# Performance work log

Hardware: AMD Instinct MI355X
Metric: run time of the kernel (lower is better)

Reference implementation:

```python
import jax, jax.numpy as jnp
import numpy as np

N = 100000   # nodes
E = 1600000  # edges
H = 150      # hidden_dim
G = 256      # num graphs in batch
L = 5        # num_layers
GATE_H = 200


def setup_inputs() -> dict:
    key = jax.random.key(0)
    ks = jax.random.split(key, 12)
    s = lambda k, shape, fan: jax.random.normal(k, shape, dtype=jnp.float32) / np.sqrt(fan)
    return {
        "x": jax.random.normal(ks[0], (N, H), dtype=jnp.float32),
        "edge_index": jax.random.randint(ks[1], (2, E), 0, N, dtype=jnp.int64),
        "batch": jnp.sort(jax.random.randint(ks[2], (N,), 0, G, dtype=jnp.int64)),
        "W": s(ks[3], (L, H, H), H),              # GatedGraphConv per-layer weight
        "w_ih": s(ks[4], (3 * H, H), H),           # GRUCell input weights (r,z,n)
        "w_hh": s(ks[5], (3 * H, H), H),
        "b_ih": jnp.zeros((3 * H,), jnp.float32),
        "b_hh": jnp.zeros((3 * H,), jnp.float32),
        "gw1": s(ks[6], (H, GATE_H), H),           # gate_nn Linear(150,200)
        "gb1": jnp.zeros((GATE_H,), jnp.float32),
        "gw2": s(ks[7], (GATE_H, 1), GATE_H),      # gate_nn Linear(200,1)
        "gb2": jnp.zeros((1,), jnp.float32),
    }


def _gru_cell(m, h, w_ih, w_hh, b_ih, b_hh):
    gi = m @ w_ih.T + b_ih   # [N, 3H]
    gh = h @ w_hh.T + b_hh
    ir, iz, inn = jnp.split(gi, 3, axis=-1)
    hr, hz, hn = jnp.split(gh, 3, axis=-1)
    r = jax.nn.sigmoid(ir + hr)
    z = jax.nn.sigmoid(iz + hz)
    n = jnp.tanh(inn + r * hn)
    return (1.0 - z) * n + z * h


def reference(x, edge_index, batch, W, w_ih, w_hh, b_ih, b_hh, gw1, gb1, gw2, gb2):
    src, dst = edge_index[0], edge_index[1]
    h = x
    # GatedGraphConv: per layer, linear transform, scatter_add aggregation, GRU update
    for i in range(L):
        m = h @ W[i]                                   # [N, H]
        agg = jax.ops.segment_sum(m[src], dst, num_segments=N)  # scatter_add over edges
        h = _gru_cell(agg, h, w_ih, w_hh, b_ih, b_hh)
    # GlobalAttention readout
    gate = jnp.tanh(h @ gw1 + gb1) @ gw2 + gb2          # [N, 1]
    gmax = jax.ops.segment_max(gate, batch, num_segments=G)    # [G, 1]
    gate = jnp.exp(gate - gmax[batch])
    gsum = jax.ops.segment_sum(gate, batch, num_segments=G)    # [G, 1]
    gate = gate / (gsum[batch] + 1e-16)                 # segment softmax
    out = jax.ops.segment_sum(gate * h, batch, num_segments=G)  # [G, H]
    return out, gate
```

## Files before the change

kernel.cpp:

```cpp
#include <hip/hip_runtime.h>
#include <math.h>

#define NN 100000
#define NE 1600000
#define H 150
#define NG 256
#define NL 5
#define GH 200
#define HS 160
#define LS 168
#define CHN 1563
#define SNB 98

typedef unsigned short u16;
typedef unsigned int   u32;
typedef __attribute__((ext_vector_type(8))) short bf16x8;
typedef __attribute__((ext_vector_type(4))) float f32x4;

__device__ __forceinline__ float bf2f(u32 lo16){ u32 t = lo16 << 16; return __builtin_bit_cast(float, t); }
__device__ __forceinline__ u16 f2bf(float f){
  u32 u = __builtin_bit_cast(u32, f);
  u += 0x7fffu + ((u >> 16) & 1u);
  return (u16)(u >> 16);
}
__device__ __forceinline__ u32 pack2(float a, float b){ return (u32)f2bf(a) | ((u32)f2bf(b) << 16); }
__device__ __forceinline__ float fast_sig(float x){
  float e = __expf(-x);
  return __builtin_amdgcn_rcpf(1.f + e);
}
__device__ __forceinline__ float fast_tanh(float x){
  float cx = fminf(fmaxf(x, -15.f), 15.f);
  float e = __expf(2.f*cx);
  return (e - 1.f) * __builtin_amdgcn_rcpf(e + 1.f);
}

__global__ void k_hist(const int* __restrict__ ed, int* __restrict__ cnt){
  int e = blockIdx.x*256 + threadIdx.x;
  if (e < NE) atomicAdd(&cnt[ed[e]], 1);
}

__global__ __launch_bounds__(256) void k_scan1(const int* __restrict__ cnt, int* __restrict__ part){
  __shared__ int red[256];
  const int b = blockIdx.x, tid = threadIdx.x;
  const int base = b*1024;
  int s = 0;
  #pragma unroll
  for (int i = 0; i < 4; ++i){
    int idx = base + tid + i*256;
    s += (idx < NN) ? cnt[idx] : 0;
  }
  red[tid] = s; __syncthreads();
  for (int st = 128; st >= 1; st >>= 1){
    if (tid < st) red[tid] += red[tid+st];
    __syncthreads();
  }
  if (tid == 0) part[b] = red[0];
}

__global__ void k_scan2(int* __restrict__ part){
  const int t = threadIdx.x;
  int v0 = (2*t   < SNB) ? part[2*t]   : 0;
  int v1 = (2*t+1 < SNB) ? part[2*t+1] : 0;
  int s = v0 + v1, x = s;
  #pragma unroll
  for (int off = 1; off < 64; off <<= 1){
    int tt = __shfl_up(x, off);
    if (t >= off) x += tt;
  }
  int excl = x - s;
  if (2*t   < SNB) part[2*t]   = excl;
  if (2*t+1 < SNB) part[2*t+1] = excl + v0;
}

__global__ __launch_bounds__(1024) void k_scan3(const int* __restrict__ cnt,
        const int* __restrict__ part, int* __restrict__ rowptr, int* __restrict__ cursor){
  __shared__ int wsum[16];
  const int b = blockIdx.x, tid = threadIdx.x;
  const int wid = tid >> 6, lane = tid & 63;
  const int idx = b*1024 + tid;
  int v = (idx < NN) ? cnt[idx] : 0;
  int x = v;
  #pragma unroll
  for (int off = 1; off < 64; off <<= 1){
    int t = __shfl_up(x, off);
    if (lane >= off) x += t;
  }
  if (lane == 63) wsum[wid] = x;
  __syncthreads();
  if (tid < 16){
    int s = wsum[tid];
    int y = s;
    #pragma unroll
    for (int off = 1; off < 16; off <<= 1){
      int t = __shfl_up(y, off);
      if (tid >= off) y += t;
    }
    wsum[tid] = y - s;
  }
  __syncthreads();
  if (idx < NN){
    int incl = part[b] + wsum[wid] + x;
    rowptr[idx+1] = incl;
    cursor[idx]   = incl - v;
  }
  if (idx == 0) rowptr[0] = 0;
}

__global__ void k_fill(const int* __restrict__ es, const int* __restrict__ ed,
                       int* __restrict__ cursor, int* __restrict__ csr){
  int e = blockIdx.x*256 + threadIdx.x;
  if (e < NE){
    int pos = atomicAdd(&cursor[ed[e]], 1);
    csr[pos] = es[e];
  }
}

__global__ __launch_bounds__(256) void k_wc(const float* __restrict__ W,
        const float* __restrict__ wih, float* __restrict__ Wc){
  int idx = blockIdx.x*256 + threadIdx.x;
  if (idx >= NL*H*450) return;
  int l = idx / (H*450);
  int rem = idx - l*H*450;
  int k = rem / 450;
  int j = rem - k*450;
  const float* Wr = W   + (size_t)l*H*H + (size_t)k*H;
  const float* wr = wih + (size_t)j*H;
  float acc = 0.f;
  for (int t = 0; t < H; ++t) acc = fmaf(Wr[t], wr[t], acc);
  Wc[idx] = acc;
}

__global__ void k_packi(const float* __restrict__ Wc, short* __restrict__ wbi){
  int idx = blockIdx.x*256 + threadIdx.x;
  int li = idx & 511;
  int q = idx >> 9;
  int mat = q % 3; q /= 3;
  int ks = q % 5;  q /= 5;
  int ct = q % 10; int l = q / 10;
  int lane = li >> 3, j = li & 7;
  int k = ks*32 + ((lane >> 4) << 3) + j;
  int col = ct*16 + (lane & 15);
  float v = (k < H && col < H) ? Wc[(size_t)l*H*450 + (size_t)k*450 + mat*H + col] : 0.f;
  wbi[idx] = (short)f2bf(v);
}

__global__ void k_packh(const float* __restrict__ whh, short* __restrict__ wbh){
  int idx = blockIdx.x*256 + threadIdx.x;
  int li = idx & 511;
  int q = idx >> 9;
  int mat = q % 3; q /= 3;
  int ks = q % 5;  int ct = q / 5;
  int lane = li >> 3, j = li & 7;
  int k = ks*32 + ((lane >> 4) << 3) + j;
  int col = ct*16 + (lane & 15);
  float v = (k < H && col < H) ? whh[(size_t)(mat*H + col)*H + k] : 0.f;
  wbh[idx] = (short)f2bf(v);
}

__global__ void k_packg(const float* __restrict__ gw1, short* __restrict__ gw1b){
  int idx = blockIdx.x*256 + threadIdx.x;
  int li = idx & 511;
  int q = idx >> 9;
  int ks = q % 5;  int ct = q / 5;
  int lane = li >> 3, j = li & 7;
  int k = ks*32 + ((lane >> 4) << 3) + j;
  int col = ct*16 + (lane & 15);
  float v = (k < H && col < GH) ? gw1[(size_t)k*GH + col] : 0.f;
  gw1b[idx] = (short)f2bf(v);
}

__global__ void k_cvt(const float* __restrict__ x, short* __restrict__ hb){
  int idx = blockIdx.x*256 + threadIdx.x;
  if (idx >= NN*80) return;
  int n = idx / 80, c2 = idx - n*80;
  int c = c2*2;
  float lo = (c   < H) ? x[(size_t)n*H + c]   : 0.f;
  float hi = (c+1 < H) ? x[(size_t)n*H + c+1] : 0.f;
  ((u32*)hb)[idx] = (u32)f2bf(lo) | ((u32)f2bf(hi) << 16);
}

__global__ __launch_bounds__(256) void k_gather(const short* __restrict__ hb,
        const int* __restrict__ rowptr, const int* __restrict__ csr,
        short* __restrict__ aggb){
  const int lane = threadIdx.x & 63;
  const int n = blockIdx.x*4 + (threadIdx.x >> 6);
  if (n >= NN) return;
  const int s0 = rowptr[n], s1 = rowptr[n+1];
  const u32* h32 = (const u32*)hb;
  const bool ext = lane < 16;
  float x0=0.f, x1=0.f, y0=0.f, y1=0.f;
  int j = s0;
  for (; j + 3 < s1; j += 4){
    const u32* r0 = h32 + (size_t)csr[j]*80;
    const u32* r1 = h32 + (size_t)csr[j+1]*80;
    const u32* r2 = h32 + (size_t)csr[j+2]*80;
    const u32* r3 = h32 + (size_t)csr[j+3]*80;
    u32 v0 = r0[lane], v1 = r1[lane], v2 = r2[lane], v3 = r3[lane];
    u32 u0=0,u1=0,u2=0,u3=0;
    if (ext){ u0 = r0[64+lane]; u1 = r1[64+lane]; u2 = r2[64+lane]; u3 = r3[64+lane]; }
    x0 += bf2f(v0 & 0xffffu) + bf2f(v1 & 0xffffu) + bf2f(v2 & 0xffffu) + bf2f(v3 & 0xffffu);
    x1 += bf2f(v0 >> 16)     + bf2f(v1 >> 16)     + bf2f(v2 >> 16)     + bf2f(v3 >> 16);
    if (ext){
      y0 += bf2f(u0 & 0xffffu) + bf2f(u1 & 0xffffu) + bf2f(u2 & 0xffffu) + bf2f(u3 & 0xffffu);
      y1 += bf2f(u0 >> 16)     + bf2f(u1 >> 16)     + bf2f(u2 >> 16)     + bf2f(u3 >> 16);
    }
  }
  for (; j < s1; ++j){
    const u32* r0 = h32 + (size_t)csr[j]*80;
    u32 v0 = r0[lane];
    x0 += bf2f(v0 & 0xffffu); x1 += bf2f(v0 >> 16);
    if (ext){
      u32 u0 = r0[64+lane];
      y0 += bf2f(u0 & 0xffffu); y1 += bf2f(u0 >> 16);
    }
  }
  u32* o = (u32*)aggb + (size_t)n*80;
  o[lane] = pack2(x0, x1);
  if (ext) o[64+lane] = pack2(y0, y1);
}

__global__ __launch_bounds__(256, 2) void k_gru(
    const short* __restrict__ aggb, const short* __restrict__ hbc,
    short* __restrict__ hbn,
    const short* __restrict__ wbi_l, const short* __restrict__ wbh,
    const float* __restrict__ bih, const float* __restrict__ bhh){
  __shared__ short sA[64*LS];
  __shared__ short sH[64*LS];
  __shared__ short sB[30*512];
  const int tid = threadIdx.x;
  const int w = tid >> 6, lane = tid & 63;
  const int l16 = lane & 15, g = lane >> 4, g8 = g*8;
  const int row0 = blockIdx.x*64;

  for (int i = tid; i < 64*20; i += 256){
    int r = i/20, c = i - r*20;
    int gr = row0 + r;
    bf16x8 va = {0,0,0,0,0,0,0,0}, vh = {0,0,0,0,0,0,0,0};
    if (gr < NN){
      va = *(const bf16x8*)&aggb[(size_t)gr*HS + c*8];
      vh = *(const bf16x8*)&hbc [(size_t)gr*HS + c*8];
    }
    *(bf16x8*)&sA[r*LS + c*8] = va;
    *(bf16x8*)&sH[r*LS + c*8] = vh;
  }

  bf16x8 pr[8];
  #pragma unroll
  for (int k2 = 0; k2 < 8; ++k2){
    int u = tid + k2*256;
    if (u < 1920){
      int s = u >> 6, e = u & 63;
      const short* src = (s < 15) ? (wbi_l + s*512 + e*8)
                                  : (wbh  + (s-15)*512 + e*8);
      pr[k2] = *(const bf16x8*)src;
    }
  }

  for (int ct = 0; ct < 10; ++ct){
    __syncthreads();
    #pragma unroll
    for (int k2 = 0; k2 < 8; ++k2){
      int u = tid + k2*256;
      if (u < 1920) *(bf16x8*)&sB[u*8] = pr[k2];
    }
    __syncthreads();
    if (ct < 9){
      const int cto = (ct+1)*7680;
      #pragma unroll
      for (int k2 = 0; k2 < 8; ++k2){
        int u = tid + k2*256;
        if (u < 1920){
          int s = u >> 6, e = u & 63;
          const short* src = (s < 15) ? (wbi_l + cto + s*512 + e*8)
                                      : (wbh  + cto + (s-15)*512 + e*8);
          pr[k2] = *(const bf16x8*)src;
        }
      }
    }

    const int col = ct*16 + l16;
    const bool cv = col < H;
    float bir = cv ? bih[col] : 0.f, biz = cv ? bih[H+col] : 0.f, bin_ = cv ? bih[2*H+col] : 0.f;
    float bhr = cv ? bhh[col] : 0.f, bhz = cv ? bhh[H+col] : 0.f, bhn  = cv ? bhh[2*H+col] : 0.f;

    f32x4 a0={0,0,0,0},a1={0,0,0,0},a2={0,0,0,0},a3={0,0,0,0},a4={0,0,0,0},a5={0,0,0,0};
    const int lr = w*16 + l16;
    #pragma unroll
    for (int ks = 0; ks < 5; ++ks){
      bf16x8 aA = *(const bf16x8*)&sA[lr*LS + ks*32 + g8];
      bf16x8 aH = *(const bf16x8*)&sH[lr*LS + ks*32 + g8];
      bf16x8 b0 = *(const bf16x8*)&sB[(ks*3+0)*512 + lane*8];
      bf16x8 b1 = *(const bf16x8*)&sB[(ks*3+1)*512 + lane*8];
      bf16x8 b2 = *(const bf16x8*)&sB[(ks*3+2)*512 + lane*8];
      bf16x8 c0 = *(const bf16x8*)&sB[(15+ks*3+0)*512 + lane*8];
      bf16x8 c1 = *(const bf16x8*)&sB[(15+ks*3+1)*512 + lane*8];
      bf16x8 c2 = *(const bf16x8*)&sB[(15+ks*3+2)*512 + lane*8];
      a0 = __builtin_amdgcn_mfma_f32_16x16x32_bf16(aA, b0, a0, 0,0,0);
      a1 = __builtin_amdgcn_mfma_f32_16x16x32_bf16(aA, b1, a1, 0,0,0);
      a2 = __builtin_amdgcn_mfma_f32_16x16x32_bf16(aA, b2, a2, 0,0,0);
      a3 = __builtin_amdgcn_mfma_f32_16x16x32_bf16(aH, c0, a3, 0,0,0);
      a4 = __builtin_amdgcn_mfma_f32_16x16x32_bf16(aH, c1, a4, 0,0,0);
      a5 = __builtin_amdgcn_mfma_f32_16x16x32_bf16(aH, c2, a5, 0,0,0);
    }
    if (cv){
      #pragma unroll
      for (int r = 0; r < 4; ++r){
        int lrow = w*16 + g*4 + r;
        int grow = row0 + lrow;
        if (grow < NN){
          float rr = fast_sig(a0[r]+bir + a3[r]+bhr);
          float zz = fast_sig(a1[r]+biz + a4[r]+bhz);
          float nn = fast_tanh(a2[r]+bin_ + rr*(a5[r]+bhn));
          float hold = bf2f((u32)(u16)sH[lrow*LS + col]);
          float hnew = (1.f-zz)*nn + zz*hold;
          hbn[(size_t)grow*HS + col] = (short)f2bf(hnew);
        }
      }
    }
  }
}

__global__ __launch_bounds__(256) void k_gatepre(const short* __restrict__ hb,
      const short* __restrict__ gw1b, const float* __restrict__ gb1,
      const float* __restrict__ gw2, const float* __restrict__ gb2,
      float* __restrict__ gbuf){
  __shared__ short sh[64*LS];
  __shared__ float part[4][4][4][4];
  const int tid = threadIdx.x;
  const int w = tid >> 6, lane = tid & 63;
  const int l16 = lane & 15, g = lane >> 4, g8 = g*8;
  const int chunk = blockIdx.x, row0 = chunk*64;

  for (int i = tid; i < 64*20; i += 256){
    int r = i/20, c = i - r*20;
    int gr = row0 + r;
    bf16x8 v = {0,0,0,0,0,0,0,0};
    if (gr < NN) v = *(const bf16x8*)&hb[(size_t)gr*HS + c*8];
    *(bf16x8*)&sh[r*LS + c*8] = v;
  }
  __syncthreads();

  float acc[4][4];
  #pragma unroll
  for (int rt=0; rt<4; ++rt){
    #pragma unroll
    for (int r=0; r<4; ++r) acc[rt][r] = 0.f;
  }
  for (int ct = w; ct < 13; ct += 4){
    bf16x8 B[5];
    const short* p = gw1b + (size_t)(ct*5)*512 + lane*8;
    #pragma unroll
    for (int ks = 0; ks < 5; ++ks) B[ks] = *(const bf16x8*)&p[ks*512];
    int col = ct*16 + l16;
    bool cv = col < GH;
    float g2 = cv ? gw2[col] : 0.f;
    float b1 = cv ? gb1[col] : 0.f;
    #pragma unroll
    for (int rt = 0; rt < 4; ++rt){
      f32x4 d = {0,0,0,0};
      #pragma unroll
      for (int ks = 0; ks < 5; ++ks){
        bf16x8 aH = *(const bf16x8*)&sh[(rt*16 + l16)*LS + ks*32 + g8];
        d = __builtin_amdgcn_mfma_f32_16x16x32_bf16(aH, B[ks], d, 0,0,0);
      }
      if (cv){
        #pragma unroll
        for (int r = 0; r < 4; ++r) acc[rt][r] += fast_tanh(d[r] + b1) * g2;
      }
    }
  }
  #pragma unroll
  for (int rt = 0; rt < 4; ++rt){
    #pragma unroll
    for (int r = 0; r < 4; ++r){
      float v = acc[rt][r];
      v += __shfl_xor(v, 1); v += __shfl_xor(v, 2);
      v += __shfl_xor(v, 4); v += __shfl_xor(v, 8);
      if (l16 == 0) part[w][rt][g][r] = v;
    }
  }
  __syncthreads();
  if (tid < 64){
    int rt = tid >> 4, gg = (tid >> 2) & 3, r = tid & 3;
    int grow = row0 + tid;
    if (grow < NN)
      gbuf[grow] = part[0][rt][gg][r] + part[1][rt][gg][r]
                 + part[2][rt][gg][r] + part[3][rt][gg][r] + gb2[0];
  }
}

__global__ __launch_bounds__(256) void k_readout(float* __restrict__ gatebuf,
    const short* __restrict__ hb, const int* __restrict__ batch,
    float* __restrict__ out, float* __restrict__ gate_out){
  const int g = blockIdx.x;
  const int tid = threadIdx.x;
  int lo=0, hi=NN;
  while (lo<hi){ int mid=(lo+hi)>>1; if (batch[mid] < g) lo=mid+1; else hi=mid; }
  const int start = lo;
  hi = NN;
  while (lo<hi){ int mid=(lo+hi)>>1; if (batch[mid] < g+1) lo=mid+1; else hi=mid; }
  const int end = lo;

  __shared__ float red[256];
  __shared__ float s_max, s_inv;
  float mx = -INFINITY;
  for (int n = start+tid; n < end; n += 256) mx = fmaxf(mx, gatebuf[n]);
  red[tid]=mx; __syncthreads();
  for (int s=128; s>=1; s>>=1){ if (tid<s) red[tid]=fmaxf(red[tid],red[tid+s]); __syncthreads(); }
  if (tid==0) s_max = red[0];
  __syncthreads();
  const float gmax = s_max;
  float sum = 0.f;
  for (int n = start+tid; n < end; n += 256){
    float e = expf(gatebuf[n]-gmax);
    gatebuf[n] = e;
    sum += e;
  }
  red[tid]=sum; __syncthreads();
  for (int s=128; s>=1; s>>=1){ if (tid<s) red[tid]+=red[tid+s]; __syncthreads(); }
  if (tid==0) s_inv = 1.0f/(red[0] + 1e-16f);
  __syncthreads();
  const float inv = s_inv;
  for (int n = start+tid; n < end; n += 256) gate_out[n] = gatebuf[n]*inv;
  if (tid < 80){
    const u32* h32 = (const u32*)hb;
    float acc0 = 0.f, acc1 = 0.f;
    for (int n = start; n < end; ++n){
      u32 v = h32[(size_t)n*80 + tid];
      float gv = gatebuf[n];
      acc0 = fmaf(gv, bf2f(v & 0xffffu), acc0);
      acc1 = fmaf(gv, bf2f(v >> 16),     acc1);
    }
    int c0 = 2*tid, c1 = 2*tid + 1;
    if (c0 < H) out[g*H + c0] = acc0*inv;
    if (c1 < H) out[g*H + c1] = acc1*inv;
  }
}

extern "C" void kernel_launch(void* const* d_in, const int* in_sizes, int n_in,
                              void* d_out, int out_size, void* d_ws, size_t ws_size,
                              hipStream_t stream) {
  (void)in_sizes; (void)n_in; (void)out_size; (void)ws_size;
  const float* x    = (const float*)d_in[0];
  const int*   eidx = (const int*)d_in[1];
  const int*   batch= (const int*)d_in[2];
  const float* W    = (const float*)d_in[3];
  const float* wih  = (const float*)d_in[4];
  const float* whh  = (const float*)d_in[5];
  const float* bih  = (const float*)d_in[6];
  const float* bhh  = (const float*)d_in[7];
  const float* gw1  = (const float*)d_in[8];
  const float* gb1  = (const float*)d_in[9];
  const float* gw2  = (const float*)d_in[10];
  const float* gb2  = (const float*)d_in[11];

  float* out      = (float*)d_out;
  float* gate_out = out + NG*H;

  char* p = (char*)d_ws;
  float* gbuf  = (float*)p;  p += (size_t)NN*4;
  float* Wc    = (float*)p;  p += (size_t)NL*H*450*4;
  short* hb0   = (short*)p;  p += (size_t)NN*HS*2;
  short* hb1   = (short*)p;  p += (size_t)NN*HS*2;
  short* aggb  = (short*)p;  p += (size_t)NN*HS*2;
  short* wbi   = (short*)p;  p += (size_t)NL*76800*2;
  short* wbh   = (short*)p;  p += (size_t)76800*2;
  short* gw1b  = (short*)p;  p += (size_t)33280*2;
  int*   cnt   = (int*)p;    p += (size_t)NN*4;
  int*   rowptr= (int*)p;    p += (size_t)(NN+1)*4;
  int*   cursor= (int*)p;    p += (size_t)NN*4;
  int*   csr   = (int*)p;    p += (size_t)NE*4;
  int*   spart = (int*)p;    p += (size_t)SNB*4;

  const int* esrc = eidx;
  const int* edst = eidx + NE;

  hipMemsetAsync(cnt, 0, sizeof(int)*NN, stream);
  k_hist<<<(NE+255)/256, 256, 0, stream>>>(edst, cnt);
  k_scan1<<<SNB, 256, 0, stream>>>(cnt, spart);
  k_scan2<<<1, 64, 0, stream>>>(spart);
  k_scan3<<<SNB, 1024, 0, stream>>>(cnt, spart, rowptr, cursor);
  k_fill<<<(NE+255)/256, 256, 0, stream>>>(esrc, edst, cursor, csr);

  k_wc   <<<(NL*H*450+255)/256, 256, 0, stream>>>(W, wih, Wc);
  k_packi<<<1500, 256, 0, stream>>>(Wc, wbi);
  k_packh<<<300,  256, 0, stream>>>(whh, wbh);
  k_packg<<<130,  256, 0, stream>>>(gw1, gw1b);

  k_cvt<<<(NN*80+255)/256, 256, 0, stream>>>(x, hb0);

  for (int l = 0; l < NL; ++l){
    short* cur  = (l & 1) ? hb1 : hb0;
    short* next = (l & 1) ? hb0 : hb1;
    k_gather<<<NN/4, 256, 0, stream>>>(cur, rowptr, csr, aggb);
    k_gru<<<CHN, 256, 0, stream>>>(aggb, cur, next,
                                   wbi + (size_t)l*76800, wbh, bih, bhh);
  }
  k_gatepre<<<CHN, 256, 0, stream>>>(hb1, gw1b, gb1, gw2, gb2, gbuf);
  k_readout<<<NG, 256, 0, stream>>>(gbuf, hb1, batch, out, gate_out);
}
```

Before: 1.307 ms.

## Keep GRU A-fragments in registers with 128-row tiles; unroll gather by eight

The GRU kernel no longer stages aggregated and hidden tiles in shared memory. Each wave loads its own MFMA A-fragments straight from global memory into registers and covers 32 rows instead of 16. Each weight tile staged in LDS is therefore reused for twice as many rows, and the grid is halved. The old hidden value is now re-read from global memory in the epilogue. The gather kernel's neighbour loop is unrolled from 4 to 8 to keep more loads in flight. Register pressure rises in both kernels, which may lower occupancy.

```diff
diff --git a/kernel.cpp b/kernel.cpp
--- a/kernel.cpp
+++ b/kernel.cpp
@@ -10,6 +10,7 @@
 #define HS 160
 #define LS 168
 #define CHN 1563
+#define CH2 782
 #define SNB 98
 
 typedef unsigned short u16;
@@ -190,19 +191,31 @@
   const bool ext = lane < 16;
   float x0=0.f, x1=0.f, y0=0.f, y1=0.f;
   int j = s0;
-  for (; j + 3 < s1; j += 4){
+  for (; j + 7 < s1; j += 8){
     const u32* r0 = h32 + (size_t)csr[j]*80;
     const u32* r1 = h32 + (size_t)csr[j+1]*80;
     const u32* r2 = h32 + (size_t)csr[j+2]*80;
     const u32* r3 = h32 + (size_t)csr[j+3]*80;
+    const u32* r4 = h32 + (size_t)csr[j+4]*80;
+    const u32* r5 = h32 + (size_t)csr[j+5]*80;
+    const u32* r6 = h32 + (size_t)csr[j+6]*80;
+    const u32* r7 = h32 + (size_t)csr[j+7]*80;
     u32 v0 = r0[lane], v1 = r1[lane], v2 = r2[lane], v3 = r3[lane];
-    u32 u0=0,u1=0,u2=0,u3=0;
-    if (ext){ u0 = r0[64+lane]; u1 = r1[64+lane]; u2 = r2[64+lane]; u3 = r3[64+lane]; }
-    x0 += bf2f(v0 & 0xffffu) + bf2f(v1 & 0xffffu) + bf2f(v2 & 0xffffu) + bf2f(v3 & 0xffffu);
-    x1 += bf2f(v0 >> 16)     + bf2f(v1 >> 16)     + bf2f(v2 >> 16)     + bf2f(v3 >> 16);
+    u32 v4 = r4[lane], v5 = r5[lane], v6 = r6[lane], v7 = r7[lane];
+    u32 u0=0,u1=0,u2=0,u3=0,u4=0,u5=0,u6=0,u7=0;
     if (ext){
-      y0 += bf2f(u0 & 0xffffu) + bf2f(u1 & 0xffffu) + bf2f(u2 & 0xffffu) + bf2f(u3 & 0xffffu);
-      y1 += bf2f(u0 >> 16)     + bf2f(u1 >> 16)     + bf2f(u2 >> 16)     + bf2f(u3 >> 16);
+      u0 = r0[64+lane]; u1 = r1[64+lane]; u2 = r2[64+lane]; u3 = r3[64+lane];
+      u4 = r4[64+lane]; u5 = r5[64+lane]; u6 = r6[64+lane]; u7 = r7[64+lane];
+    }
+    x0 += bf2f(v0 & 0xffffu) + bf2f(v1 & 0xffffu) + bf2f(v2 & 0xffffu) + bf2f(v3 & 0xffffu)
+        + bf2f(v4 & 0xffffu) + bf2f(v5 & 0xffffu) + bf2f(v6 & 0xffffu) + bf2f(v7 & 0xffffu);
+    x1 += bf2f(v0 >> 16) + bf2f(v1 >> 16) + bf2f(v2 >> 16) + bf2f(v3 >> 16)
+        + bf2f(v4 >> 16) + bf2f(v5 >> 16) + bf2f(v6 >> 16) + bf2f(v7 >> 16);
+    if (ext){
+      y0 += bf2f(u0 & 0xffffu) + bf2f(u1 & 0xffffu) + bf2f(u2 & 0xffffu) + bf2f(u3 & 0xffffu)
+          + bf2f(u4 & 0xffffu) + bf2f(u5 & 0xffffu) + bf2f(u6 & 0xffffu) + bf2f(u7 & 0xffffu);
+      y1 += bf2f(u0 >> 16) + bf2f(u1 >> 16) + bf2f(u2 >> 16) + bf2f(u3 >> 16)
+          + bf2f(u4 >> 16) + bf2f(u5 >> 16) + bf2f(u6 >> 16) + bf2f(u7 >> 16);
     }
   }
   for (; j < s1; ++j){
@@ -224,24 +237,26 @@
     short* __restrict__ hbn,
     const short* __restrict__ wbi_l, const short* __restrict__ wbh,
     const float* __restrict__ bih, const float* __restrict__ bhh){
-  __shared__ short sA[64*LS];
-  __shared__ short sH[64*LS];
   __shared__ short sB[30*512];
   const int tid = threadIdx.x;
   const int w = tid >> 6, lane = tid & 63;
   const int l16 = lane & 15, g = lane >> 4, g8 = g*8;
-  const int row0 = blockIdx.x*64;
-
-  for (int i = tid; i < 64*20; i += 256){
-    int r = i/20, c = i - r*20;
-    int gr = row0 + r;
-    bf16x8 va = {0,0,0,0,0,0,0,0}, vh = {0,0,0,0,0,0,0,0};
-    if (gr < NN){
-      va = *(const bf16x8*)&aggb[(size_t)gr*HS + c*8];
-      vh = *(const bf16x8*)&hbc [(size_t)gr*HS + c*8];
-    }
-    *(bf16x8*)&sA[r*LS + c*8] = va;
-    *(bf16x8*)&sH[r*LS + c*8] = vh;
+  const int row0 = blockIdx.x*128 + w*32;
+
+  bf16x8 fA[2][5], fH[2][5];
+  #pragma unroll
+  for (int t = 0; t < 2; ++t){
+    const int r = row0 + t*16 + l16;
+    const bool rv = r < NN;
+    #pragma unroll
+    for (int ks = 0; ks < 5; ++ks){
+      bf16x8 va = {0,0,0,0,0,0,0,0}, vh = {0,0,0,0,0,0,0,0};
+      if (rv){
+        va = *(const bf16x8*)&aggb[(size_t)r*HS + ks*32 + g8];
+        vh = *(const bf16x8*)&hbc [(size_t)r*HS + ks*32 + g8];
+      }
+      fA[t][ks] = va; fH[t][ks] = vh;
+    }
   }
 
   bf16x8 pr[8];
@@ -280,40 +295,48 @@
 
     const int col = ct*16 + l16;
     const bool cv = col < H;
-    float bir = cv ? bih[col] : 0.f, biz = cv ? bih[H+col] : 0.f, bin_ = cv ? bih[2*H+col] : 0.f;
-    float bhr = cv ? bhh[col] : 0.f, bhz = cv ? bhh[H+col] : 0.f, bhn  = cv ? bhh[2*H+col] : 0.f;
-
-    f32x4 a0={0,0,0,0},a1={0,0,0,0},a2={0,0,0,0},a3={0,0,0,0},a4={0,0,0,0},a5={0,0,0,0};
-    const int lr = w*16 + l16;
+    const float bir = cv ? bih[col] : 0.f, biz = cv ? bih[H+col] : 0.f, bin_ = cv ? bih[2*H+col] : 0.f;
+    const float bhr = cv ? bhh[col] : 0.f, bhz = cv ? bhh[H+col] : 0.f, bhn  = cv ? bhh[2*H+col] : 0.f;
+
+    f32x4 ai[2][3], ah[2][3];
+    #pragma unroll
+    for (int t = 0; t < 2; ++t)
+      #pragma unroll
+      for (int m = 0; m < 3; ++m){ ai[t][m] = (f32x4){0,0,0,0}; ah[t][m] = (f32x4){0,0,0,0}; }
+
     #pragma unroll
     for (int ks = 0; ks < 5; ++ks){
-      bf16x8 aA = *(const bf16x8*)&sA[lr*LS + ks*32 + g8];
-      bf16x8 aH = *(const bf16x8*)&sH[lr*LS + ks*32 + g8];
-      bf16x8 b0 = *(const bf16x8*)&sB[(ks*3+0)*512 + lane*8];
-      bf16x8 b1 = *(const bf16x8*)&sB[(ks*3+1)*512 + lane*8];
-      bf16x8 b2 = *(const bf16x8*)&sB[(ks*3+2)*512 + lane*8];
-      bf16x8 c0 = *(const bf16x8*)&sB[(15+ks*3+0)*512 + lane*8];
-      bf16x8 c1 = *(const bf16x8*)&sB[(15+ks*3+1)*512 + lane*8];
-      bf16x8 c2 = *(const bf16x8*)&sB[(15+ks*3+2)*512 + lane*8];
-      a0 = __builtin_amdgcn_mfma_f32_16x16x32_bf16(aA, b0, a0, 0,0,0);
-      a1 = __builtin_amdgcn_mfma_f32_16x16x32_bf16(aA, b1, a1, 0,0,0);
-      a2 = __builtin_amdgcn_mfma_f32_16x16x32_bf16(aA, b2, a2, 0,0,0);
-      a3 = __builtin_amdgcn_mfma_f32_16x16x32_bf16(aH, c0, a3, 0,0,0);
-      a4 = __builtin_amdgcn_mfma_f32_16x16x32_bf16(aH, c1, a4, 0,0,0);
-      a5 = __builtin_amdgcn_mfma_f32_16x16x32_bf16(aH, c2, a5, 0,0,0);
-    }
+      bf16x8 bi0 = *(const bf16x8*)&sB[(ks*3+0)*512 + lane*8];
+      bf16x8 bi1 = *(const bf16x8*)&sB[(ks*3+1)*512 + lane*8];
+      bf16x8 bi2 = *(const bf16x8*)&sB[(ks*3+2)*512 + lane*8];
+      bf16x8 bh0 = *(const bf16x8*)&sB[(15+ks*3+0)*512 + lane*8];
+      bf16x8 bh1 = *(const bf16x8*)&sB[(15+ks*3+1)*512 + lane*8];
+      bf16x8 bh2 = *(const bf16x8*)&sB[(15+ks*3+2)*512 + lane*8];
+      #pragma unroll
+      for (int t = 0; t < 2; ++t){
+        ai[t][0] = __builtin_amdgcn_mfma_f32_16x16x32_bf16(fA[t][ks], bi0, ai[t][0], 0,0,0);
+        ai[t][1] = __builtin_amdgcn_mfma_f32_16x16x32_bf16(fA[t][ks], bi1, ai[t][1], 0,0,0);
+        ai[t][2] = __builtin_amdgcn_mfma_f32_16x16x32_bf16(fA[t][ks], bi2, ai[t][2], 0,0,0);
+        ah[t][0] = __builtin_amdgcn_mfma_f32_16x16x32_bf16(fH[t][ks], bh0, ah[t][0], 0,0,0);
+        ah[t][1] = __builtin_amdgcn_mfma_f32_16x16x32_bf16(fH[t][ks], bh1, ah[t][1], 0,0,0);
+        ah[t][2] = __builtin_amdgcn_mfma_f32_16x16x32_bf16(fH[t][ks], bh2, ah[t][2], 0,0,0);
+      }
+    }
+
     if (cv){
       #pragma unroll
-      for (int r = 0; r < 4; ++r){
-        int lrow = w*16 + g*4 + r;
-        int grow = row0 + lrow;
-        if (grow < NN){
-          float rr = fast_sig(a0[r]+bir + a3[r]+bhr);
-          float zz = fast_sig(a1[r]+biz + a4[r]+bhz);
-          float nn = fast_tanh(a2[r]+bin_ + rr*(a5[r]+bhn));
-          float hold = bf2f((u32)(u16)sH[lrow*LS + col]);
-          float hnew = (1.f-zz)*nn + zz*hold;
-          hbn[(size_t)grow*HS + col] = (short)f2bf(hnew);
+      for (int t = 0; t < 2; ++t){
+        #pragma unroll
+        for (int r = 0; r < 4; ++r){
+          int grow = row0 + t*16 + g*4 + r;
+          if (grow < NN){
+            float rr = fast_sig(ai[t][0][r]+bir + ah[t][0][r]+bhr);
+            float zz = fast_sig(ai[t][1][r]+biz + ah[t][1][r]+bhz);
+            float nn = fast_tanh(ai[t][2][r]+bin_ + rr*(ah[t][2][r]+bhn));
+            float hold = bf2f((u32)(u16)hbc[(size_t)grow*HS + col]);
+            float hnew = (1.f-zz)*nn + zz*hold;
+            hbn[(size_t)grow*HS + col] = (short)f2bf(hnew);
+          }
         }
       }
     }
@@ -493,7 +516,7 @@
     short* cur  = (l & 1) ? hb1 : hb0;
     short* next = (l & 1) ? hb0 : hb1;
     k_gather<<<NN/4, 256, 0, stream>>>(cur, rowptr, csr, aggb);
-    k_gru<<<CHN, 256, 0, stream>>>(aggb, cur, next,
+    k_gru<<<CH2, 256, 0, stream>>>(aggb, cur, next,
                                    wbi + (size_t)l*76800, wbh, bih, bhh);
   }
   k_gatepre<<<CHN, 256, 0, stream>>>(hb1, gw1b, gb1, gw2, gb2, gbuf);
```

Measured after the change: 1.259 ms. 3.6% less time.
